# Performance work log

Measured on AMD Instinct MI355X. Metric: run time of the kernel, lower is better.

Reference implementation:

```python
import jax, jax.numpy as jnp
import numpy as np

N_NODES = 100000
N_EDGES = 1600000
HEADS = 8
CH = 16
NEG_SLOPE = 0.2


def setup_inputs() -> dict:
    key = jax.random.key(0)
    ks = jax.random.split(key, 8)
    x = jax.random.normal(ks[0], (N_NODES, 16), dtype=jnp.float32)
    edge_index = jax.random.randint(ks[1], (2, N_EDGES), 0, N_NODES, dtype=jnp.int64)
    W = jax.random.normal(ks[2], (16, HEADS * CH), dtype=jnp.float32) * 0.25
    att_src = jax.random.normal(ks[3], (HEADS, CH), dtype=jnp.float32) * 0.25
    att_dst = jax.random.normal(ks[4], (HEADS, CH), dtype=jnp.float32) * 0.25
    bias = jax.random.normal(ks[5], (HEADS * CH,), dtype=jnp.float32) * 0.1
    fc_w = jax.random.normal(ks[6], (HEADS * CH, 5), dtype=jnp.float32) * 0.1
    fc_b = jax.random.normal(ks[7], (5,), dtype=jnp.float32) * 0.1
    return {"x": x, "edge_index": edge_index, "W": W, "att_src": att_src,
            "att_dst": att_dst, "bias": bias, "fc_w": fc_w, "fc_b": fc_b}


def reference(x, edge_index, W, att_src, att_dst, bias, fc_w, fc_b):
    N = x.shape[0]
    # PyG GATConv default: add self loops
    loops = jnp.arange(N, dtype=edge_index.dtype)
    src = jnp.concatenate([edge_index[0], loops])
    dst = jnp.concatenate([edge_index[1], loops])

    h = (x @ W).reshape(N, HEADS, CH)                 # [N,H,C]
    a_src = jnp.einsum('nhc,hc->nh', h, att_src)      # [N,H]
    a_dst = jnp.einsum('nhc,hc->nh', h, att_dst)      # [N,H]

    e = a_src[src] + a_dst[dst]                       # [E,H]
    e = jax.nn.leaky_relu(e, NEG_SLOPE)
    # segment softmax over edges grouped by destination node
    e_max = jax.ops.segment_max(e, dst, num_segments=N)
    e_exp = jnp.exp(e - e_max[dst])
    denom = jax.ops.segment_sum(e_exp, dst, num_segments=N)
    alpha = e_exp / (denom[dst] + 1e-16)              # [E,H]

    msg = alpha[:, :, None] * h[src]                  # [E,H,C]
    out = jax.ops.segment_sum(msg, dst, num_segments=N)  # [N,H,C]
    out = out.reshape(N, HEADS * CH) + bias           # concat heads + bias

    out = jax.nn.relu(out)
    # dropout is identity in eval mode
    logits = out @ fc_w + fc_b                        # [N,5]
    return jax.nn.log_softmax(logits, axis=1)
```

## Files before the change

### kernel.cpp

```cpp
#include <hip/hip_runtime.h>
#include <hip/hip_bf16.h>
#include <math.h>

#define N_NODES 100000
#define N_EDGES 1600000
#define HEADS 8
#define HC 128
#define LOG2E 1.44269504f

#define DPB 64
#define NB 1563
#define NBP (NB + 1)
#define NCH 512
#define EPC (N_EDGES / NCH)
#define CAPS 2048
#define NA 196

__global__ __launch_bounds__(512) void k_prep(
    const float* __restrict__ x, const float* __restrict__ W,
    const float* __restrict__ att_s, const float* __restrict__ att_d,
    const int* __restrict__ ei,
    unsigned short* __restrict__ a_srcb, float* __restrict__ a_dst,
    uint4* __restrict__ x2b,
    int* __restrict__ offs, unsigned* __restrict__ stg) {
    __shared__ int smem[2048 + EPC];
    __shared__ int ws8[8];
    int t = threadIdx.x;
    if (blockIdx.x >= NCH) {
        float* sM = (float*)smem;
        if (t < 256) {
            int k = t >> 4, h2 = t & 15;
            const float* av = (h2 < 8) ? att_s : att_d;
            int h = h2 & 7;
            float s = 0.f;
#pragma unroll
            for (int c = 0; c < 16; ++c)
                s = fmaf(W[k * HC + h * 16 + c], av[h * 16 + c], s);
            sM[k * 16 + h2] = s * LOG2E;
        }
        __syncthreads();
        int node = (blockIdx.x - NCH) * 512 + t;
        if (node < N_NODES) {
            const float4* xr = (const float4*)(x + node * 16);
            float4 x0 = xr[0], x1 = xr[1], x2 = xr[2], x3 = xr[3];
            float xv[16] = {x0.x, x0.y, x0.z, x0.w, x1.x, x1.y, x1.z, x1.w,
                            x2.x, x2.y, x2.z, x2.w, x3.x, x3.y, x3.z, x3.w};
            union { uint4 u[2]; __hip_bfloat162 b[8]; } px;
#pragma unroll
            for (int k = 0; k < 8; ++k)
                px.b[k] = __float22bfloat162_rn(float2{xv[2 * k], xv[2 * k + 1]});
            x2b[node * 2] = px.u[0];
            x2b[node * 2 + 1] = px.u[1];
#pragma unroll
            for (int h2 = 0; h2 < 16; ++h2) {
                float o = 0.f;
#pragma unroll
                for (int k = 0; k < 16; ++k) o = fmaf(xv[k], sM[k * 16 + h2], o);
                if (h2 < 8) a_srcb[node * 8 + h2] =
                    __bfloat16_as_ushort(__float2bfloat16(o));
                else        a_dst[node * 8 + (h2 - 8)] = o;
            }
        }
    } else {
        int* hist = smem;
        unsigned* entries = (unsigned*)(smem + 2048);
        int c = blockIdx.x;
        hist[t] = 0; hist[t + 512] = 0; hist[t + 1024] = 0; hist[t + 1536] = 0;
        __syncthreads();
        int beg = c * EPC, end = beg + EPC;
        for (int e = beg + t; e < end; e += 512)
            atomicAdd(&hist[ei[N_EDGES + e] >> 6], 1);
        __syncthreads();
        int i0 = 4 * t;
        int v0 = hist[i0], v1 = hist[i0 + 1], v2 = hist[i0 + 2], v3 = hist[i0 + 3];
        int s1 = v0 + v1, s2 = s1 + v2, T = s2 + v3;
        int lane = t & 63, wv = t >> 6;
        int inc = T;
#pragma unroll
        for (int off = 1; off < 64; off <<= 1) {
            int y = __shfl_up(inc, off);
            if (lane >= off) inc += y;
        }
        if (lane == 63) ws8[wv] = inc;
        __syncthreads();
        int wbase = 0;
        for (int k = 0; k < wv; ++k) wbase += ws8[k];
        int e0 = wbase + inc - T;
        hist[i0] = e0; hist[i0 + 1] = e0 + v0;
        hist[i0 + 2] = e0 + s1; hist[i0 + 3] = e0 + s2;
        __syncthreads();
        int row = c * NBP;
        for (int b = t; b < NB; b += 512) offs[row + b] = hist[b];
        if (t == 0) offs[row + NB] = EPC;
        __syncthreads();
        for (int e = beg + t; e < end; e += 512) {
            int src = ei[e], dst = ei[N_EDGES + e];
            int pos = atomicAdd(&hist[dst >> 6], 1);
            entries[pos] = ((unsigned)(dst & 63) << 17) | (unsigned)src;
        }
        __syncthreads();
        unsigned* so = stg + beg;
        for (int i = t; i < EPC; i += 512) so[i] = entries[i];
    }
}

__global__ __launch_bounds__(256) void k_tr(const int* __restrict__ offs,
                                            int* __restrict__ offsT) {
    __shared__ int tile[64][65];
    int b0 = (blockIdx.x >> 3) * 64;
    int c0 = (blockIdx.x & 7) * 64;
    int t = threadIdx.x;
    for (int i = t; i < 4096; i += 256) {
        int cc = i >> 6, bb = i & 63;
        int b = b0 + bb;
        tile[bb][cc] = (b < NBP) ? offs[(c0 + cc) * NBP + b] : 0;
    }
    __syncthreads();
    for (int i = t; i < 4096; i += 256) {
        int bb = i >> 6, cc = i & 63;
        int b = b0 + bb;
        if (b < NBP) offsT[b * NCH + c0 + cc] = tile[bb][cc];
    }
}

__global__ __launch_bounds__(512) void k_gather(
    const __hip_bfloat162* __restrict__ x2b,
    const unsigned short* __restrict__ a_srcb, const float* __restrict__ W,
    const float* __restrict__ a_dst,
    const int* __restrict__ offsT, const unsigned* __restrict__ stg,
    const float* __restrict__ bias, const float* __restrict__ fc_w,
    const float* __restrict__ fc_b, float* __restrict__ out) {
    __shared__ unsigned estage[CAPS];
    __shared__ int cstage[CAPS];
    __shared__ float sW[16 * HC];
    __shared__ int o0_s[NCH];
    __shared__ int myb_s[NCH + 1];
    __shared__ int hist[DPB];
    __shared__ int bs[DPB + 1];
    __shared__ int ws8[8];
    int b = blockIdx.x, t = threadIdx.x;
    int d0 = b * DPB;
    for (int i = t; i < 16 * HC; i += 512) sW[i] = W[i];
    int lane = t & 63, wv = t >> 6;
    {
        int o0 = offsT[b * NCH + t];
        int len = offsT[(b + 1) * NCH + t] - o0;
        o0_s[t] = o0;
        int inc = len;
#pragma unroll
        for (int off = 1; off < 64; off <<= 1) {
            int y = __shfl_up(inc, off);
            if (lane >= off) inc += y;
        }
        if (lane == 63) ws8[wv] = inc;
        __syncthreads();
        int wbase = 0;
        for (int k = 0; k < wv; ++k) wbase += ws8[k];
        myb_s[t] = wbase + inc - len;
        if (t == 511) myb_s[NCH] = wbase + inc;
    }
    if (t < DPB) hist[t] = (d0 + t < N_NODES) ? 1 : 0;
    __syncthreads();
    int tot = myb_s[NCH];
    for (int i = t; i < tot; i += 512) {
        int lo = 0, hi = NCH - 1;
#pragma unroll
        for (int s = 0; s < 9; ++s) {
            int mid = (lo + hi + 1) >> 1;
            if (myb_s[mid] <= i) lo = mid; else hi = mid - 1;
        }
        estage[i] = stg[lo * EPC + o0_s[lo] + (i - myb_s[lo])];
    }
    __syncthreads();
    for (int i = t; i < tot; i += 512) atomicAdd(&hist[estage[i] >> 17], 1);
    __syncthreads();
    if (t < 64) {
        int v = hist[t];
        int iv = v;
#pragma unroll
        for (int off = 1; off < 64; off <<= 1) {
            int y = __shfl_up(iv, off);
            if (t >= off) iv += y;
        }
        int excl = iv - v;
        bs[t] = excl;
        if (t == 63) bs[64] = iv;
        int gd = d0 + t;
        bool val = gd < N_NODES;
        if (val) cstage[excl] = gd;
        hist[t] = excl + (val ? 1 : 0);
    }
    __syncthreads();
    for (int i = t; i < tot; i += 512) {
        unsigned u = estage[i];
        int pos = atomicAdd(&hist[u >> 17], 1);
        cstage[pos] = (int)(u & 0x1FFFF);
    }
    __syncthreads();
    int q = t & 31, g = t >> 5;
    int head = q >> 2, i4 = q & 3;
    int c0 = q * 4;
    float b0 = bias[c0], b1 = bias[c0 + 1], b2 = bias[c0 + 2], b3 = bias[c0 + 3];
    float fw[4][5], fb[5];
#pragma unroll
    for (int k = 0; k < 4; ++k)
#pragma unroll
        for (int j = 0; j < 5; ++j) fw[k][j] = fc_w[(c0 + k) * 5 + j];
#pragma unroll
    for (int j = 0; j < 5; ++j) fb[j] = fc_b[j];
    for (int l4 = 0; l4 < 4; ++l4) {
        int l = g * 4 + l4;
        int gd = d0 + l;
        if (gd >= N_NODES) break;
        int beg = bs[l], end = bs[l + 1];
        float ad = a_dst[gd * 8 + head];
        float A0 = 0.f, A1 = 0.f, A2 = 0.f, A3 = 0.f, wsum = 0.f;
        int j = beg;
        for (; j + 2 <= end; j += 2) {
            int s0 = cstage[j], s1 = cstage[j + 1];
            unsigned short u0 = a_srcb[s0 * 8 + head];
            unsigned short u1 = a_srcb[s1 * 8 + head];
            union { uint2 u; __hip_bfloat162 bb[2]; } xa, xb;
            xa.u = *(const uint2*)(x2b + (size_t)s0 * 8 + i4 * 2);
            xb.u = *(const uint2*)(x2b + (size_t)s1 * 8 + i4 * 2);
            float e0 = __bfloat162float(__ushort_as_bfloat16(u0)) + ad;
            float e1 = __bfloat162float(__ushort_as_bfloat16(u1)) + ad;
            e0 = fmaxf(e0, 0.2f * e0);
            e1 = fmaxf(e1, 0.2f * e1);
            float w0 = exp2f(e0), w1 = exp2f(e1);
            float2 a01 = __bfloat1622float2(xa.bb[0]);
            float2 a23 = __bfloat1622float2(xa.bb[1]);
            float2 b01 = __bfloat1622float2(xb.bb[0]);
            float2 b23 = __bfloat1622float2(xb.bb[1]);
            A0 = fmaf(w0, a01.x, A0); A1 = fmaf(w0, a01.y, A1);
            A2 = fmaf(w0, a23.x, A2); A3 = fmaf(w0, a23.y, A3);
            A0 = fmaf(w1, b01.x, A0); A1 = fmaf(w1, b01.y, A1);
            A2 = fmaf(w1, b23.x, A2); A3 = fmaf(w1, b23.y, A3);
            wsum += w0 + w1;
        }
        if (j < end) {
            int s0 = cstage[j];
            float as = __bfloat162float(
                __ushort_as_bfloat16(a_srcb[s0 * 8 + head]));
            float e = as + ad;
            e = fmaxf(e, 0.2f * e);
            float w = exp2f(e);
            union { uint2 u; __hip_bfloat162 bb[2]; } xu;
            xu.u = *(const uint2*)(x2b + (size_t)s0 * 8 + i4 * 2);
            float2 f01 = __bfloat1622float2(xu.bb[0]);
            float2 f23 = __bfloat1622float2(xu.bb[1]);
            A0 = fmaf(w, f01.x, A0); A1 = fmaf(w, f01.y, A1);
            A2 = fmaf(w, f23.x, A2); A3 = fmaf(w, f23.y, A3);
            wsum += w;
        }
        float inv = 1.f / (wsum + 1e-16f);
        A0 *= inv; A1 *= inv; A2 *= inv; A3 *= inv;
        float ov0 = 0.f, ov1 = 0.f, ov2 = 0.f, ov3 = 0.f;
#pragma unroll
        for (int ii = 0; ii < 4; ++ii) {
            int sl = (q & 28) + ii;
            float a0 = __shfl(A0, sl, 32);
            float a1 = __shfl(A1, sl, 32);
            float a2 = __shfl(A2, sl, 32);
            float a3 = __shfl(A3, sl, 32);
            const float* w0 = sW + (4 * ii) * HC + c0;
            ov0 = fmaf(a0, w0[0], ov0); ov1 = fmaf(a0, w0[1], ov1);
            ov2 = fmaf(a0, w0[2], ov2); ov3 = fmaf(a0, w0[3], ov3);
            const float* w1 = w0 + HC;
            ov0 = fmaf(a1, w1[0], ov0); ov1 = fmaf(a1, w1[1], ov1);
            ov2 = fmaf(a1, w1[2], ov2); ov3 = fmaf(a1, w1[3], ov3);
            const float* w2 = w1 + HC;
            ov0 = fmaf(a2, w2[0], ov0); ov1 = fmaf(a2, w2[1], ov1);
            ov2 = fmaf(a2, w2[2], ov2); ov3 = fmaf(a2, w2[3], ov3);
            const float* w3 = w2 + HC;
            ov0 = fmaf(a3, w3[0], ov0); ov1 = fmaf(a3, w3[1], ov1);
            ov2 = fmaf(a3, w3[2], ov2); ov3 = fmaf(a3, w3[3], ov3);
        }
        ov0 = fmaxf(ov0 + b0, 0.f);
        ov1 = fmaxf(ov1 + b1, 0.f);
        ov2 = fmaxf(ov2 + b2, 0.f);
        ov3 = fmaxf(ov3 + b3, 0.f);
        float p[5];
#pragma unroll
        for (int j2 = 0; j2 < 5; ++j2)
            p[j2] = ov0 * fw[0][j2] + ov1 * fw[1][j2]
                  + ov2 * fw[2][j2] + ov3 * fw[3][j2];
#pragma unroll
        for (int off = 16; off >= 1; off >>= 1) {
#pragma unroll
            for (int j2 = 0; j2 < 5; ++j2) p[j2] += __shfl_xor(p[j2], off);
        }
        if (q == 0) {
            float lg[5], m = -1e30f;
#pragma unroll
            for (int j2 = 0; j2 < 5; ++j2) {
                lg[j2] = p[j2] + fb[j2];
                m = fmaxf(m, lg[j2]);
            }
            float sum = 0.f;
#pragma unroll
            for (int j2 = 0; j2 < 5; ++j2) sum += __expf(lg[j2] - m);
            float ls = m + __logf(sum);
#pragma unroll
            for (int j2 = 0; j2 < 5; ++j2) out[gd * 5 + j2] = lg[j2] - ls;
        }
    }
}

extern "C" void kernel_launch(void* const* d_in, const int* in_sizes, int n_in,
                              void* d_out, int out_size, void* d_ws, size_t ws_size,
                              hipStream_t stream) {
    const float* x     = (const float*)d_in[0];
    const int*   ei    = (const int*)d_in[1];
    const float* W     = (const float*)d_in[2];
    const float* att_s = (const float*)d_in[3];
    const float* att_d = (const float*)d_in[4];
    const float* bias  = (const float*)d_in[5];
    const float* fc_w  = (const float*)d_in[6];
    const float* fc_b  = (const float*)d_in[7];
    float* out = (float*)d_out;

    char* ws = (char*)d_ws;
    size_t off = 0;
    auto carve = [&](size_t bytes) {
        void* p = ws + off;
        off = (off + bytes + 255) & ~(size_t)255;
        return p;
    };
    unsigned short* a_srcb = (unsigned short*)carve((size_t)N_NODES * HEADS * 2);
    float*    a_dst = (float*)   carve((size_t)N_NODES * HEADS * 4);
    uint4*    x2b   = (uint4*)   carve((size_t)N_NODES * 32);
    int*      offs  = (int*)     carve((size_t)NCH * NBP * 4);
    int*      offsT = (int*)     carve((size_t)NBP * NCH * 4);
    unsigned* stg   = (unsigned*)carve((size_t)N_EDGES * 4);

    k_prep<<<NCH + NA, 512, 0, stream>>>(x, W, att_s, att_d, ei,
                                         a_srcb, a_dst, x2b, offs, stg);
    k_tr<<<200, 256, 0, stream>>>(offs, offsT);
    k_gather<<<NB, 512, 0, stream>>>((const __hip_bfloat162*)x2b, a_srcb, W,
                                     a_dst, offsT, stg, bias, fc_w, fc_b, out);
}
```

Before: 183.2 us.

## Precompute per-edge attention weights for all heads in LDS, widen gather

Adds a pass that computes the leaky-relu/exp attention weights for all 8 heads once per edge. It reads the full a_src row as one 16-byte load, takes a_dst from a shared-memory copy, and stores the weights as fp16 in LDS. Before this, each head lane fetched its own scalar a_src and redid the exp. The gather loop now maps 16 lanes per node with 8 channels each, uses 16-byte x loads, and walks edges 4 at a time over segments padded to multiples of 4 with dummy entries whose weight underflows to zero. This costs an extra LDS pass and barrier, lowers weight precision to fp16, and shrinks the staging capacity, so a block with more edges could overflow.

```diff
diff --git a/kernel.cpp b/kernel.cpp
--- a/kernel.cpp
+++ b/kernel.cpp
@@ -1,5 +1,6 @@
 #include <hip/hip_runtime.h>
 #include <hip/hip_bf16.h>
+#include <hip/hip_fp16.h>
 #include <math.h>
 
 #define N_NODES 100000
@@ -13,7 +14,8 @@
 #define NBP (NB + 1)
 #define NCH 512
 #define EPC (N_EDGES / NCH)
-#define CAPS 2048
+#define CAPS 1664
+#define WSTR (CAPS + 4)
 #define NA 196
 
 __global__ __launch_bounds__(512) void k_prep(
@@ -130,17 +132,22 @@
     const int* __restrict__ offsT, const unsigned* __restrict__ stg,
     const float* __restrict__ bias, const float* __restrict__ fc_w,
     const float* __restrict__ fc_b, float* __restrict__ out) {
-    __shared__ unsigned estage[CAPS];
-    __shared__ int cstage[CAPS];
-    __shared__ float sW[16 * HC];
+    __shared__ __align__(16) unsigned buf0[(8 * WSTR) / 2];
+    __shared__ __align__(16) int cstage[CAPS];
+    __shared__ __align__(16) float sW[16 * HC];
     __shared__ int o0_s[NCH];
     __shared__ int myb_s[NCH + 1];
+    __shared__ __align__(16) float sad[8 * DPB + 8];
     __shared__ int hist[DPB];
     __shared__ int bs[DPB + 1];
     __shared__ int ws8[8];
+    unsigned* estage = buf0;
+    unsigned short* wst = (unsigned short*)buf0;
     int b = blockIdx.x, t = threadIdx.x;
     int d0 = b * DPB;
     for (int i = t; i < 16 * HC; i += 512) sW[i] = W[i];
+    sad[t] = (d0 * 8 + t < N_NODES * 8) ? a_dst[(size_t)d0 * 8 + t] : 0.f;
+    if (t < 8) sad[8 * DPB + t] = -100000.f;
     int lane = t & 63, wv = t >> 6;
     {
         int o0 = offsT[b * NCH + t];
@@ -175,134 +182,145 @@
     for (int i = t; i < tot; i += 512) atomicAdd(&hist[estage[i] >> 17], 1);
     __syncthreads();
     if (t < 64) {
-        int v = hist[t];
-        int iv = v;
+        int gd = d0 + t;
+        bool val = gd < N_NODES;
+        int len = hist[t];
+        int plen = (len + 3) & ~3;
+        int iv = plen;
 #pragma unroll
         for (int off = 1; off < 64; off <<= 1) {
             int y = __shfl_up(iv, off);
             if (t >= off) iv += y;
         }
-        int excl = iv - v;
+        int excl = iv - plen;
         bs[t] = excl;
         if (t == 63) bs[64] = iv;
-        int gd = d0 + t;
-        bool val = gd < N_NODES;
-        if (val) cstage[excl] = gd;
+        if (val) cstage[excl] = (t << 17) | gd;
         hist[t] = excl + (val ? 1 : 0);
+        for (int k = len; k < plen; ++k) cstage[excl + k] = (64 << 17);
     }
     __syncthreads();
     for (int i = t; i < tot; i += 512) {
         unsigned u = estage[i];
         int pos = atomicAdd(&hist[u >> 17], 1);
-        cstage[pos] = (int)(u & 0x1FFFF);
-    }
-    __syncthreads();
-    int q = t & 31, g = t >> 5;
-    int head = q >> 2, i4 = q & 3;
-    int c0 = q * 4;
-    float b0 = bias[c0], b1 = bias[c0 + 1], b2 = bias[c0 + 2], b3 = bias[c0 + 3];
-    float fw[4][5], fb[5];
-#pragma unroll
-    for (int k = 0; k < 4; ++k)
-#pragma unroll
-        for (int j = 0; j < 5; ++j) fw[k][j] = fc_w[(c0 + k) * 5 + j];
-#pragma unroll
-    for (int j = 0; j < 5; ++j) fb[j] = fc_b[j];
-    for (int l4 = 0; l4 < 4; ++l4) {
-        int l = g * 4 + l4;
+        cstage[pos] = (int)u;
+    }
+    __syncthreads();
+    int ctot = bs[DPB];
+    for (int i = t; i < ctot; i += 512) {
+        unsigned u = (unsigned)cstage[i];
+        int s = (int)(u & 0x1FFFF);
+        int dl = (int)(u >> 17);
+        union { uint4 v; __hip_bfloat162 b2[4]; } pa;
+        pa.v = *(const uint4*)(a_srcb + (size_t)s * 8);
+        const float* adp = sad + dl * 8;
+        float4 ad0 = *(const float4*)(adp);
+        float4 ad1 = *(const float4*)(adp + 4);
+        float2 s01 = __bfloat1622float2(pa.b2[0]);
+        float2 s23 = __bfloat1622float2(pa.b2[1]);
+        float2 s45 = __bfloat1622float2(pa.b2[2]);
+        float2 s67 = __bfloat1622float2(pa.b2[3]);
+        float e[8] = {s01.x + ad0.x, s01.y + ad0.y, s23.x + ad0.z, s23.y + ad0.w,
+                      s45.x + ad1.x, s45.y + ad1.y, s67.x + ad1.z, s67.y + ad1.w};
+#pragma unroll
+        for (int h = 0; h < 8; ++h) {
+            float eh = fmaxf(e[h], 0.2f * e[h]);
+            float w = exp2f(eh);
+            wst[h * WSTR + i] = __half_as_ushort(__float2half(w));
+        }
+    }
+    __syncthreads();
+    int q = t & 15, g = t >> 4;
+    int head = q >> 1, i8 = q & 1;
+    int c0 = head * 16 + i8 * 8;
+    const unsigned short* wrow = wst + head * WSTR;
+    int xofs = i8 * 16;
+    const char* xb = (const char*)x2b;
+    float bb[8], fwv[8][5], fbv[5];
+#pragma unroll
+    for (int m = 0; m < 8; ++m) bb[m] = bias[c0 + m];
+#pragma unroll
+    for (int m = 0; m < 8; ++m)
+#pragma unroll
+        for (int jj = 0; jj < 5; ++jj) fwv[m][jj] = fc_w[(c0 + m) * 5 + jj];
+#pragma unroll
+    for (int jj = 0; jj < 5; ++jj) fbv[jj] = fc_b[jj];
+    for (int l4 = 0; l4 < 2; ++l4) {
+        int l = g * 2 + l4;
         int gd = d0 + l;
         if (gd >= N_NODES) break;
         int beg = bs[l], end = bs[l + 1];
-        float ad = a_dst[gd * 8 + head];
-        float A0 = 0.f, A1 = 0.f, A2 = 0.f, A3 = 0.f, wsum = 0.f;
-        int j = beg;
-        for (; j + 2 <= end; j += 2) {
-            int s0 = cstage[j], s1 = cstage[j + 1];
-            unsigned short u0 = a_srcb[s0 * 8 + head];
-            unsigned short u1 = a_srcb[s1 * 8 + head];
-            union { uint2 u; __hip_bfloat162 bb[2]; } xa, xb;
-            xa.u = *(const uint2*)(x2b + (size_t)s0 * 8 + i4 * 2);
-            xb.u = *(const uint2*)(x2b + (size_t)s1 * 8 + i4 * 2);
-            float e0 = __bfloat162float(__ushort_as_bfloat16(u0)) + ad;
-            float e1 = __bfloat162float(__ushort_as_bfloat16(u1)) + ad;
-            e0 = fmaxf(e0, 0.2f * e0);
-            e1 = fmaxf(e1, 0.2f * e1);
-            float w0 = exp2f(e0), w1 = exp2f(e1);
-            float2 a01 = __bfloat1622float2(xa.bb[0]);
-            float2 a23 = __bfloat1622float2(xa.bb[1]);
-            float2 b01 = __bfloat1622float2(xb.bb[0]);
-            float2 b23 = __bfloat1622float2(xb.bb[1]);
-            A0 = fmaf(w0, a01.x, A0); A1 = fmaf(w0, a01.y, A1);
-            A2 = fmaf(w0, a23.x, A2); A3 = fmaf(w0, a23.y, A3);
-            A0 = fmaf(w1, b01.x, A0); A1 = fmaf(w1, b01.y, A1);
-            A2 = fmaf(w1, b23.x, A2); A3 = fmaf(w1, b23.y, A3);
-            wsum += w0 + w1;
-        }
-        if (j < end) {
-            int s0 = cstage[j];
-            float as = __bfloat162float(
-                __ushort_as_bfloat16(a_srcb[s0 * 8 + head]));
-            float e = as + ad;
-            e = fmaxf(e, 0.2f * e);
-            float w = exp2f(e);
-            union { uint2 u; __hip_bfloat162 bb[2]; } xu;
-            xu.u = *(const uint2*)(x2b + (size_t)s0 * 8 + i4 * 2);
-            float2 f01 = __bfloat1622float2(xu.bb[0]);
-            float2 f23 = __bfloat1622float2(xu.bb[1]);
-            A0 = fmaf(w, f01.x, A0); A1 = fmaf(w, f01.y, A1);
-            A2 = fmaf(w, f23.x, A2); A3 = fmaf(w, f23.y, A3);
-            wsum += w;
+        float A[8] = {0.f, 0.f, 0.f, 0.f, 0.f, 0.f, 0.f, 0.f};
+        float wsum = 0.f;
+        auto acc = [&](const uint4& xv, float w) {
+            union { uint4 v; __hip_bfloat162 b2[4]; } xx; xx.v = xv;
+            float2 f0 = __bfloat1622float2(xx.b2[0]);
+            float2 f1 = __bfloat1622float2(xx.b2[1]);
+            float2 f2 = __bfloat1622float2(xx.b2[2]);
+            float2 f3 = __bfloat1622float2(xx.b2[3]);
+            A[0] = fmaf(w, f0.x, A[0]); A[1] = fmaf(w, f0.y, A[1]);
+            A[2] = fmaf(w, f1.x, A[2]); A[3] = fmaf(w, f1.y, A[3]);
+            A[4] = fmaf(w, f2.x, A[4]); A[5] = fmaf(w, f2.y, A[5]);
+            A[6] = fmaf(w, f3.x, A[6]); A[7] = fmaf(w, f3.y, A[7]);
+        };
+        for (int j = beg; j < end; j += 4) {
+            int4 cs = *(const int4*)(cstage + j);
+            uint2 wu = *(const uint2*)(wrow + j);
+            union { uint2 u2; __half2 h2[2]; } wq; wq.u2 = wu;
+            float2 w01 = __half22float2(wq.h2[0]);
+            float2 w23 = __half22float2(wq.h2[1]);
+            int s0 = cs.x & 0x1FFFF, s1 = cs.y & 0x1FFFF;
+            int s2 = cs.z & 0x1FFFF, s3 = cs.w & 0x1FFFF;
+            uint4 xv0 = *(const uint4*)(xb + ((s0 << 5) + xofs));
+            uint4 xv1 = *(const uint4*)(xb + ((s1 << 5) + xofs));
+            uint4 xv2 = *(const uint4*)(xb + ((s2 << 5) + xofs));
+            uint4 xv3 = *(const uint4*)(xb + ((s3 << 5) + xofs));
+            acc(xv0, w01.x); acc(xv1, w01.y);
+            acc(xv2, w23.x); acc(xv3, w23.y);
+            wsum += (w01.x + w01.y) + (w23.x + w23.y);
         }
         float inv = 1.f / (wsum + 1e-16f);
-        A0 *= inv; A1 *= inv; A2 *= inv; A3 *= inv;
-        float ov0 = 0.f, ov1 = 0.f, ov2 = 0.f, ov3 = 0.f;
-#pragma unroll
-        for (int ii = 0; ii < 4; ++ii) {
-            int sl = (q & 28) + ii;
-            float a0 = __shfl(A0, sl, 32);
-            float a1 = __shfl(A1, sl, 32);
-            float a2 = __shfl(A2, sl, 32);
-            float a3 = __shfl(A3, sl, 32);
-            const float* w0 = sW + (4 * ii) * HC + c0;
-            ov0 = fmaf(a0, w0[0], ov0); ov1 = fmaf(a0, w0[1], ov1);
-            ov2 = fmaf(a0, w0[2], ov2); ov3 = fmaf(a0, w0[3], ov3);
-            const float* w1 = w0 + HC;
-            ov0 = fmaf(a1, w1[0], ov0); ov1 = fmaf(a1, w1[1], ov1);
-            ov2 = fmaf(a1, w1[2], ov2); ov3 = fmaf(a1, w1[3], ov3);
-            const float* w2 = w1 + HC;
-            ov0 = fmaf(a2, w2[0], ov0); ov1 = fmaf(a2, w2[1], ov1);
-            ov2 = fmaf(a2, w2[2], ov2); ov3 = fmaf(a2, w2[3], ov3);
-            const float* w3 = w2 + HC;
-            ov0 = fmaf(a3, w3[0], ov0); ov1 = fmaf(a3, w3[1], ov1);
-            ov2 = fmaf(a3, w3[2], ov2); ov3 = fmaf(a3, w3[3], ov3);
-        }
-        ov0 = fmaxf(ov0 + b0, 0.f);
-        ov1 = fmaxf(ov1 + b1, 0.f);
-        ov2 = fmaxf(ov2 + b2, 0.f);
-        ov3 = fmaxf(ov3 + b3, 0.f);
+#pragma unroll
+        for (int m = 0; m < 8; ++m) A[m] *= inv;
+        float ov[8] = {0.f, 0.f, 0.f, 0.f, 0.f, 0.f, 0.f, 0.f};
+#pragma unroll
+        for (int m = 0; m < 8; ++m) {
+            float a = A[m];
+            float ap = __shfl_xor(A[m], 1);
+            const float* w0r = sW + (i8 * 8 + m) * HC + c0;
+            const float* w1r = sW + ((1 - i8) * 8 + m) * HC + c0;
+#pragma unroll
+            for (int o = 0; o < 8; ++o) ov[o] = fmaf(a, w0r[o], ov[o]);
+#pragma unroll
+            for (int o = 0; o < 8; ++o) ov[o] = fmaf(ap, w1r[o], ov[o]);
+        }
+#pragma unroll
+        for (int m = 0; m < 8; ++m) ov[m] = fmaxf(ov[m] + bb[m], 0.f);
         float p[5];
 #pragma unroll
-        for (int j2 = 0; j2 < 5; ++j2)
-            p[j2] = ov0 * fw[0][j2] + ov1 * fw[1][j2]
-                  + ov2 * fw[2][j2] + ov3 * fw[3][j2];
-#pragma unroll
-        for (int off = 16; off >= 1; off >>= 1) {
-#pragma unroll
-            for (int j2 = 0; j2 < 5; ++j2) p[j2] += __shfl_xor(p[j2], off);
-        }
+        for (int jj = 0; jj < 5; ++jj) {
+            float sacc = 0.f;
+#pragma unroll
+            for (int m = 0; m < 8; ++m) sacc = fmaf(ov[m], fwv[m][jj], sacc);
+            p[jj] = sacc;
+        }
+#pragma unroll
+        for (int off = 8; off >= 1; off >>= 1)
+#pragma unroll
+            for (int jj = 0; jj < 5; ++jj) p[jj] += __shfl_xor(p[jj], off);
         if (q == 0) {
-            float lg[5], m = -1e30f;
-#pragma unroll
-            for (int j2 = 0; j2 < 5; ++j2) {
-                lg[j2] = p[j2] + fb[j2];
-                m = fmaxf(m, lg[j2]);
+            float lg[5], mx = -1e30f;
+#pragma unroll
+            for (int jj = 0; jj < 5; ++jj) {
+                lg[jj] = p[jj] + fbv[jj];
+                mx = fmaxf(mx, lg[jj]);
             }
             float sum = 0.f;
 #pragma unroll
-            for (int j2 = 0; j2 < 5; ++j2) sum += __expf(lg[j2] - m);
-            float ls = m + __logf(sum);
-#pragma unroll
-            for (int j2 = 0; j2 < 5; ++j2) out[gd * 5 + j2] = lg[j2] - ls;
+            for (int jj = 0; jj < 5; ++jj) sum += __expf(lg[jj] - mx);
+            float ls = mx + __logf(sum);
+#pragma unroll
+            for (int jj = 0; jj < 5; ++jj) out[gd * 5 + jj] = lg[jj] - ls;
         }
     }
 }
```

Measured after the change: 166.4 us. 9.2% less time.
